# Kernel optimization log

Measured on AMD Instinct MI355X. Metric: run time of the kernel, lower is better.

Reference implementation:

```python
import jax, jax.numpy as jnp
import numpy as np

B, S, D, H = 4, 2048, 1024, 16
DH = D // H

def setup_inputs() -> dict:
    key = jax.random.key(0)
    ks = jax.random.split(key, 4)
    scale = 1.0 / np.sqrt(D)
    x = jax.random.normal(ks[0], (B, S, D), dtype=jnp.float32)
    Wq = jax.random.normal(ks[1], (D, D), dtype=jnp.float32) * scale
    Wk = jax.random.normal(ks[2], (D, D), dtype=jnp.float32) * scale
    Wv = jax.random.normal(ks[3], (D, D), dtype=jnp.float32) * scale
    bq = jnp.zeros((D,), dtype=jnp.float32)
    bk = jnp.zeros((D,), dtype=jnp.float32)
    bv = jnp.zeros((D,), dtype=jnp.float32)
    # causal mask, broadcastable to [B, H, S, S]; mask==0 positions get -inf
    mask = jnp.tril(jnp.ones((S, S), dtype=bool))[None, None, :, :]
    return {"x": x, "mask": mask, "Wq": Wq, "bq": bq, "Wk": Wk, "bk": bk, "Wv": Wv, "bv": bv}

def reference(x, mask, Wq, bq, Wk, bk, Wv, bv):
    b, s, d = x.shape
    def proj(W, bias):
        # nn.Linear: x @ W.T + b, then split heads -> [b, H, s, DH]
        y = jnp.einsum('bsd,ed->bse', x, W) + bias
        return y.reshape(b, s, H, DH).transpose(0, 2, 1, 3)
    q = proj(Wq, bq)
    k = proj(Wk, bk)
    v = proj(Wv, bv)
    scores = jnp.einsum('bhqd,bhkd->bhqk', q, k) / jnp.sqrt(jnp.float32(DH))
    scores = jnp.where(mask, scores, -jnp.inf)
    attn = jax.nn.softmax(scores, axis=-1)
    out = jnp.einsum('bhqk,bhkd->bhqd', attn, v)
    return out.transpose(0, 2, 1, 3).reshape(b, s, d)
```

## Files before the change

kernel.cpp:

```cpp
#include <hip/hip_runtime.h>
#include <hip/hip_bf16.h>
#include <stdint.h>

typedef unsigned short u16;
typedef unsigned int   u32;
typedef short bf16x8 __attribute__((ext_vector_type(8)));
typedef float f32x4  __attribute__((ext_vector_type(4)));

typedef bf16x8 __attribute__((__may_alias__)) bf16x8_a;
typedef uint4  __attribute__((__may_alias__)) uint4_a;
typedef uint2  __attribute__((__may_alias__)) uint2_a;
typedef float4 __attribute__((__may_alias__)) float4_a;

#define MFMA_BF16(a,b,c) __builtin_amdgcn_mfma_f32_16x16x32_bf16((a),(b),(c),0,0,0)
#define L2E 1.44269504088896340736f

#define SEQ 2048
#define DMODEL 1024
#define NH 16
#define DH 64

__device__ __forceinline__ u32 pack_bf2(float a, float b) {
  union { __hip_bfloat162 h; u32 u; } c;
  c.h = __float22bfloat162_rn(make_float2(a, b));
  return c.u;
}

__device__ __forceinline__ u16 f2bf(float f) {
  u32 u = __builtin_bit_cast(u32, f);
  u += 0x7FFFu + ((u >> 16) & 1u);
  return (u16)(u >> 16);
}

__device__ __forceinline__ void gl_lds16(const u16* g, u16* l) {
  __builtin_amdgcn_global_load_lds(
      (const __attribute__((address_space(1))) void*)g,
      (__attribute__((address_space(3))) void*)l, 16, 0, 0);
}

__global__ __launch_bounds__(256) void cvt_x_bf16(
    const float* __restrict__ s, u16* __restrict__ d, int n8)
{
  int i = blockIdx.x * 256 + threadIdx.x;
  const int stride = gridDim.x * 256;
  for (; i < n8; i += stride) {
    const float4_a* p = (const float4_a*)(s + (size_t)i * 8);
    float4 a = p[0], b = p[1];
    uint4 o;
    o.x = pack_bf2(a.x, a.y); o.y = pack_bf2(a.z, a.w);
    o.z = pack_bf2(b.x, b.y); o.w = pack_bf2(b.z, b.w);
    *(uint4_a*)(d + (size_t)i * 8) = o;
  }
}

__global__ __launch_bounds__(256) void cvt_w_bf16(
    const float* __restrict__ wq, const float* __restrict__ wk, const float* __restrict__ wv,
    u16* __restrict__ oq, u16* __restrict__ ok, u16* __restrict__ ov)
{
  const float* s = (blockIdx.y == 0) ? wq : (blockIdx.y == 1) ? wk : wv;
  u16*         d = (blockIdx.y == 0) ? oq : (blockIdx.y == 1) ? ok : ov;
  const int i = blockIdx.x * 256 + threadIdx.x;
  const float4_a* p = (const float4_a*)(s + (size_t)i * 8);
  float4 a = p[0], b = p[1];
  uint4 o;
  o.x = pack_bf2(a.x, a.y); o.y = pack_bf2(a.z, a.w);
  o.z = pack_bf2(b.x, b.y); o.w = pack_bf2(b.z, b.w);
  *(uint4_a*)(d + (size_t)i * 8) = o;
}

__global__ __launch_bounds__(256, 4) void qkv_gemm_bf(
    const u16* __restrict__ Xb,
    const u16* __restrict__ Wqb, const u16* __restrict__ Wkb, const u16* __restrict__ Wvb,
    const float* __restrict__ Bq, const float* __restrict__ Bk, const float* __restrict__ Bv,
    u16* __restrict__ Qo, u16* __restrict__ Ko, u16* __restrict__ Vo)
{
  __shared__ u16 As[2][128 * 32];
  __shared__ u16 Bs[2][128 * 32];

  const int tid  = threadIdx.x;
  const int lane = tid & 63;
  const int wid  = tid >> 6;
  const int l16  = lane & 15;
  const int quad = lane >> 4;
  const int wm   = (wid >> 1) * 64;
  const int wn   = (wid & 1) * 64;

  const int m0 = blockIdx.x * 128;
  const int n0 = blockIdx.y * 128;
  const int pj = blockIdx.z;

  const u16*   Wb   = (pj == 0) ? Wqb : (pj == 1) ? Wkb : Wvb;
  const float* Bias = (pj == 0) ? Bq : (pj == 1) ? Bk : Bv;
  u16*         Out  = (pj == 0) ? Qo : (pj == 1) ? Ko : Vo;
  const float scale = (pj == 0) ? 0.125f : 1.0f;

  f32x4 acc[4][4];
#pragma unroll
  for (int i = 0; i < 4; i++)
#pragma unroll
    for (int j = 0; j < 4; j++) acc[i][j] = (f32x4){0.f, 0.f, 0.f, 0.f};

  const int lr = lane >> 2;
  const int lc = (lane & 3) * 8;

  const u16* Arow = Xb + (size_t)m0 * DMODEL;
  const u16* Brow = Wb + (size_t)n0 * DMODEL;

#pragma unroll
  for (int c = 0; c < 2; c++) {
    const int band = c * 64 + wid * 16;
    gl_lds16(Arow + (size_t)(band + lr) * DMODEL + lc, &As[0][band * 32]);
    gl_lds16(Brow + (size_t)(band + lr) * DMODEL + lc, &Bs[0][band * 32]);
  }

  for (int kt = 0; kt < DMODEL; kt += 32) {
    const int cur = (kt >> 5) & 1;
    __syncthreads();

    if (kt + 32 < DMODEL) {
#pragma unroll
      for (int c = 0; c < 2; c++) {
        const int band = c * 64 + wid * 16;
        gl_lds16(Arow + (size_t)(band + lr) * DMODEL + kt + 32 + lc, &As[cur ^ 1][band * 32]);
        gl_lds16(Brow + (size_t)(band + lr) * DMODEL + kt + 32 + lc, &Bs[cur ^ 1][band * 32]);
      }
    }

    bf16x8 a[4], b[4];
#pragma unroll
    for (int mt = 0; mt < 4; mt++)
      a[mt] = *(const bf16x8_a*)&As[cur][(wm + mt * 16 + l16) * 32 + quad * 8];
#pragma unroll
    for (int nt = 0; nt < 4; nt++)
      b[nt] = *(const bf16x8_a*)&Bs[cur][(wn + nt * 16 + l16) * 32 + quad * 8];
#pragma unroll
    for (int mt = 0; mt < 4; mt++)
#pragma unroll
      for (int nt = 0; nt < 4; nt++)
        acc[mt][nt] = MFMA_BF16(a[mt], b[nt], acc[mt][nt]);
  }

  if (pj == 2) {
#pragma unroll
    for (int mt = 0; mt < 4; mt++) {
#pragma unroll
      for (int nt = 0; nt < 4; nt++) {
        const int n = n0 + wn + nt * 16 + l16;
        const float bias = Bias[n];
        const int h = n >> 6, dh = n & 63;
        const int m = m0 + wm + mt * 16 + quad * 4;
        const int bb = m >> 11, ss = m & 2047;
        uint2 pk;
        pk.x = pack_bf2(acc[mt][nt][0] + bias, acc[mt][nt][1] + bias);
        pk.y = pack_bf2(acc[mt][nt][2] + bias, acc[mt][nt][3] + bias);
        *(uint2_a*)&Out[((size_t)(bb * NH + h) * DH + dh) * SEQ + ss] = pk;
      }
    }
  } else {
#pragma unroll
    for (int mt = 0; mt < 4; mt++) {
#pragma unroll
      for (int nt = 0; nt < 4; nt++) {
        const int n = n0 + wn + nt * 16 + l16;
        const float bias = Bias[n];
        const int h = n >> 6, dh = n & 63;
#pragma unroll
        for (int r = 0; r < 4; r++) {
          const int m = m0 + wm + mt * 16 + quad * 4 + r;
          const int bb = m >> 11, ss = m & 2047;
          Out[((((size_t)bb * NH + h) * SEQ + ss) << 6) + dh] = f2bf((acc[mt][nt][r] + bias) * scale);
        }
      }
    }
  }
}

__global__ __launch_bounds__(256, 2) void qkv_gemm(
    const float* __restrict__ X,
    const float* __restrict__ Wq, const float* __restrict__ Wk, const float* __restrict__ Wv,
    const float* __restrict__ Bq, const float* __restrict__ Bk, const float* __restrict__ Bv,
    u16* __restrict__ Qo, u16* __restrict__ Ko, u16* __restrict__ Vo)
{
  __shared__ u16 As[128 * 32];
  __shared__ u16 Bs[128 * 32];

  const int tid  = threadIdx.x;
  const int lane = tid & 63;
  const int wid  = tid >> 6;
  const int l16  = lane & 15;
  const int quad = lane >> 4;
  const int wm   = (wid >> 1) * 64;
  const int wn   = (wid & 1) * 64;

  const int m0 = blockIdx.x * 128;
  const int n0 = blockIdx.y * 128;
  const int pj = blockIdx.z;

  const float* W    = (pj == 0) ? Wq : (pj == 1) ? Wk : Wv;
  const float* Bias = (pj == 0) ? Bq : (pj == 1) ? Bk : Bv;
  u16*         Out  = (pj == 0) ? Qo : (pj == 1) ? Ko : Vo;
  const float scale = (pj == 0) ? 0.125f : 1.0f;

  f32x4 acc[4][4];
#pragma unroll
  for (int i = 0; i < 4; i++)
#pragma unroll
    for (int j = 0; j < 4; j++) acc[i][j] = (f32x4){0.f, 0.f, 0.f, 0.f};

  float4 gX[4], gW[4];
#pragma unroll
  for (int i = 0; i < 4; i++) {
    const int ch = i * 256 + tid;
    const int r = ch >> 3, c = ch & 7;
    gX[i] = *(const float4_a*)(X + (size_t)(m0 + r) * DMODEL + c * 4);
    gW[i] = *(const float4_a*)(W + (size_t)(n0 + r) * DMODEL + c * 4);
  }

  for (int kt = 0; kt < DMODEL; kt += 32) {
    __syncthreads();
#pragma unroll
    for (int i = 0; i < 4; i++) {
      const int ch = i * 256 + tid;
      const int r = ch >> 3, c = ch & 7;
      uint2 xp, wp;
      xp.x = pack_bf2(gX[i].x, gX[i].y);  xp.y = pack_bf2(gX[i].z, gX[i].w);
      wp.x = pack_bf2(gW[i].x, gW[i].y);  wp.y = pack_bf2(gW[i].z, gW[i].w);
      *(uint2_a*)&As[r * 32 + c * 4] = xp;
      *(uint2_a*)&Bs[r * 32 + c * 4] = wp;
    }
    __syncthreads();

    if (kt + 32 < DMODEL) {
#pragma unroll
      for (int i = 0; i < 4; i++) {
        const int ch = i * 256 + tid;
        const int r = ch >> 3, c = ch & 7;
        gX[i] = *(const float4_a*)(X + (size_t)(m0 + r) * DMODEL + kt + 32 + c * 4);
        gW[i] = *(const float4_a*)(W + (size_t)(n0 + r) * DMODEL + kt + 32 + c * 4);
      }
    }

    bf16x8 a[4], b[4];
#pragma unroll
    for (int mt = 0; mt < 4; mt++)
      a[mt] = *(const bf16x8_a*)&As[(wm + mt * 16 + l16) * 32 + quad * 8];
#pragma unroll
    for (int nt = 0; nt < 4; nt++)
      b[nt] = *(const bf16x8_a*)&Bs[(wn + nt * 16 + l16) * 32 + quad * 8];
#pragma unroll
    for (int mt = 0; mt < 4; mt++)
#pragma unroll
      for (int nt = 0; nt < 4; nt++)
        acc[mt][nt] = MFMA_BF16(a[mt], b[nt], acc[mt][nt]);
  }

  if (pj == 2) {
#pragma unroll
    for (int mt = 0; mt < 4; mt++) {
#pragma unroll
      for (int nt = 0; nt < 4; nt++) {
        const int n = n0 + wn + nt * 16 + l16;
        const float bias = Bias[n];
        const int h = n >> 6, dh = n & 63;
        const int m = m0 + wm + mt * 16 + quad * 4;
        const int bb = m >> 11, ss = m & 2047;
        uint2 pk;
        pk.x = pack_bf2(acc[mt][nt][0] + bias, acc[mt][nt][1] + bias);
        pk.y = pack_bf2(acc[mt][nt][2] + bias, acc[mt][nt][3] + bias);
        *(uint2_a*)&Out[((size_t)(bb * NH + h) * DH + dh) * SEQ + ss] = pk;
      }
    }
  } else {
#pragma unroll
    for (int mt = 0; mt < 4; mt++) {
#pragma unroll
      for (int nt = 0; nt < 4; nt++) {
        const int n = n0 + wn + nt * 16 + l16;
        const float bias = Bias[n];
        const int h = n >> 6, dh = n & 63;
#pragma unroll
        for (int r = 0; r < 4; r++) {
          const int m = m0 + wm + mt * 16 + quad * 4 + r;
          const int bb = m >> 11, ss = m & 2047;
          Out[((((size_t)bb * NH + h) * SEQ + ss) << 6) + dh] = f2bf((acc[mt][nt][r] + bias) * scale);
        }
      }
    }
  }
}

__global__ __launch_bounds__(256, 4) void flash_attn(
    const u16* __restrict__ Q, const u16* __restrict__ K, const u16* __restrict__ VT,
    float* __restrict__ O)
{
  __shared__ u16 Ks[64 * 72];
  __shared__ u16 VTs[64 * 72];
  __shared__ u16 Ps[4 * 32 * 72];

  const int tid  = threadIdx.x;
  const int lane = tid & 63;
  const int wid  = tid >> 6;
  const int l16  = lane & 15;
  const int quad = lane >> 4;

  const int idx = blockIdx.x;
  const int qt  = 15 - (idx >> 6);
  const int bh  = idx & 63;
  const int bb = bh >> 4, hh = bh & 15;
  const int qbase = qt * 128;

  const u16* Qh = Q  + (size_t)bh * (SEQ * DH);
  const u16* Kh = K  + (size_t)bh * (SEQ * DH);
  const u16* Vh = VT + (size_t)bh * (DH * SEQ);

#pragma unroll
  for (int i = 0; i < 4; i++) {
    const int ch = i * 256 + tid;
    const int r = ch >> 3, c = ch & 7;
    *(uint4_a*)&Ps[r * 72 + c * 8] = *(const uint4_a*)(Qh + (size_t)(qbase + r) * DH + c * 8);
  }
  __syncthreads();

  u16* Pw = &Ps[wid * 32 * 72];
  bf16x8 qf[2][2];
#pragma unroll
  for (int ct = 0; ct < 2; ct++)
#pragma unroll
    for (int ks = 0; ks < 2; ks++)
      qf[ct][ks] = *(const bf16x8_a*)&Pw[(ct * 16 + l16) * 72 + ks * 32 + quad * 8];

  f32x4 o[4][2];
#pragma unroll
  for (int dt = 0; dt < 4; dt++)
#pragma unroll
    for (int ct = 0; ct < 2; ct++) o[dt][ct] = (f32x4){0.f, 0.f, 0.f, 0.f};

  float mold[2] = {-1e30f, -1e30f};
  float lsum[2] = {0.f, 0.f};

  const int jmax = 2 * qt + 1;

  uint4 gK[2], gV[2];
#pragma unroll
  for (int i = 0; i < 2; i++) {
    const int ch = i * 256 + tid;
    gK[i] = *(const uint4_a*)(Kh + (size_t)(ch >> 3) * DH + (ch & 7) * 8);
    gV[i] = *(const uint4_a*)(Vh + (size_t)(ch >> 3) * SEQ + (ch & 7) * 8);
  }

  for (int j = 0; j <= jmax; j++) {
    __syncthreads();
#pragma unroll
    for (int i = 0; i < 2; i++) {
      const int ch = i * 256 + tid;
      *(uint4_a*)&Ks[(ch >> 3) * 72 + (ch & 7) * 8]  = gK[i];
      *(uint4_a*)&VTs[(ch >> 3) * 72 + (ch & 7) * 8] = gV[i];
    }
    __syncthreads();

    if (j < jmax) {
      const int kb2 = (j + 1) * 64;
#pragma unroll
      for (int i = 0; i < 2; i++) {
        const int ch = i * 256 + tid;
        gK[i] = *(const uint4_a*)(Kh + (size_t)(kb2 + (ch >> 3)) * DH + (ch & 7) * 8);
        gV[i] = *(const uint4_a*)(Vh + (size_t)(ch >> 3) * SEQ + kb2 + (ch & 7) * 8);
      }
    }

    f32x4 s[4][2];
#pragma unroll
    for (int rt = 0; rt < 4; rt++) {
      bf16x8 ka0 = *(const bf16x8_a*)&Ks[(rt * 16 + l16) * 72 + 0 + quad * 8];
      bf16x8 ka1 = *(const bf16x8_a*)&Ks[(rt * 16 + l16) * 72 + 32 + quad * 8];
#pragma unroll
      for (int ct = 0; ct < 2; ct++) {
        f32x4 c = (f32x4){0.f, 0.f, 0.f, 0.f};
        c = MFMA_BF16(ka0, qf[ct][0], c);
        c = MFMA_BF16(ka1, qf[ct][1], c);
        s[rt][ct] = c;
      }
    }

    if (j >= (qt << 1)) {
      const int kvb = j * 64;
#pragma unroll
      for (int rt = 0; rt < 4; rt++)
#pragma unroll
        for (int ct = 0; ct < 2; ct++) {
          const int ql = qbase + wid * 32 + ct * 16 + l16;
#pragma unroll
          for (int r = 0; r < 4; r++) {
            const int kvg = kvb + rt * 16 + quad * 4 + r;
            if (kvg > ql) s[rt][ct][r] = -1e30f;
          }
        }
    }

#pragma unroll
    for (int ct = 0; ct < 2; ct++) {
      float mt = -1e30f;
#pragma unroll
      for (int rt = 0; rt < 4; rt++)
#pragma unroll
        for (int r = 0; r < 4; r++) mt = fmaxf(mt, s[rt][ct][r]);
      mt = fmaxf(mt, __shfl_xor(mt, 16));
      mt = fmaxf(mt, __shfl_xor(mt, 32));
      const float mnew = fmaxf(mold[ct], mt);
      const float a = __builtin_amdgcn_exp2f((mold[ct] - mnew) * L2E);
      float ls = 0.f;
#pragma unroll
      for (int rt = 0; rt < 4; rt++)
#pragma unroll
        for (int r = 0; r < 4; r++) {
          const float p = __builtin_amdgcn_exp2f((s[rt][ct][r] - mnew) * L2E);
          s[rt][ct][r] = p;
          ls += p;
        }
      ls += __shfl_xor(ls, 16);
      ls += __shfl_xor(ls, 32);
      lsum[ct] = lsum[ct] * a + ls;
      mold[ct] = mnew;
#pragma unroll
      for (int dt = 0; dt < 4; dt++)
#pragma unroll
        for (int r = 0; r < 4; r++) o[dt][ct][r] *= a;
    }

#pragma unroll
    for (int rt = 0; rt < 4; rt++) {
#pragma unroll
      for (int ct = 0; ct < 2; ct++) {
        uint2 pk;
        pk.x = pack_bf2(s[rt][ct][0], s[rt][ct][1]);
        pk.y = pack_bf2(s[rt][ct][2], s[rt][ct][3]);
        *(uint2_a*)&Pw[(ct * 16 + l16) * 72 + rt * 16 + quad * 4] = pk;
      }
    }
    asm volatile("s_waitcnt lgkmcnt(0)" ::: "memory");

#pragma unroll
    for (int ks2 = 0; ks2 < 2; ks2++) {
      bf16x8 vt[4], pb[2];
#pragma unroll
      for (int dt = 0; dt < 4; dt++)
        vt[dt] = *(const bf16x8_a*)&VTs[(dt * 16 + l16) * 72 + ks2 * 32 + quad * 8];
#pragma unroll
      for (int ct = 0; ct < 2; ct++)
        pb[ct] = *(const bf16x8_a*)&Pw[(ct * 16 + l16) * 72 + ks2 * 32 + quad * 8];
#pragma unroll
      for (int dt = 0; dt < 4; dt++)
#pragma unroll
        for (int ct = 0; ct < 2; ct++)
          o[dt][ct] = MFMA_BF16(vt[dt], pb[ct], o[dt][ct]);
    }
  }

#pragma unroll
  for (int ct = 0; ct < 2; ct++) {
    const float inv = 1.0f / lsum[ct];
    const int qg = qbase + wid * 32 + ct * 16 + l16;
    float* orow = O + (size_t)((size_t)bb * SEQ + qg) * DMODEL + hh * 64;
#pragma unroll
    for (int dt = 0; dt < 4; dt++) {
      float4 v4;
      v4.x = o[dt][ct][0] * inv;  v4.y = o[dt][ct][1] * inv;
      v4.z = o[dt][ct][2] * inv;  v4.w = o[dt][ct][3] * inv;
      *(float4_a*)&orow[dt * 16 + quad * 4] = v4;
    }
  }
}

__global__ void paintf(float* out, int n, float v) {
  int i = blockIdx.x * 256 + threadIdx.x;
  if (i < n) out[i] = v;
}

extern "C" void kernel_launch(void* const* d_in, const int* in_sizes, int n_in,
                              void* d_out, int out_size, void* d_ws, size_t ws_size,
                              hipStream_t stream) {
  float* out = (float*)d_out;

  const size_t elems  = (size_t)4 * SEQ * DMODEL;
  const size_t welems = (size_t)DMODEL * DMODEL;
  const size_t need_old = 3 * elems * sizeof(u16);
  const size_t need_new = (4 * elems + 3 * welems) * sizeof(u16);

  if (ws_size < need_old) {
    paintf<<<(out_size + 255) / 256, 256, 0, stream>>>(out, out_size, 3.0e38f);
    return;
  }

  const float* x  = (const float*)d_in[0];
  const float* Wq = (const float*)d_in[2];
  const float* bq = (const float*)d_in[3];
  const float* Wk = (const float*)d_in[4];
  const float* bk = (const float*)d_in[5];
  const float* Wv = (const float*)d_in[6];
  const float* bv = (const float*)d_in[7];

  u16* q = (u16*)d_ws;
  u16* k = q + elems;
  u16* v = k + elems;

  if (ws_size >= need_new) {
    u16* xb  = v + elems;
    u16* wqb = xb + elems;
    u16* wkb = wqb + welems;
    u16* wvb = wkb + welems;
    cvt_x_bf16<<<2048, 256, 0, stream>>>(x, xb, (int)(elems / 8));
    cvt_w_bf16<<<dim3(512, 3), 256, 0, stream>>>(Wq, Wk, Wv, wqb, wkb, wvb);
    qkv_gemm_bf<<<dim3(64, 8, 3), 256, 0, stream>>>(xb, wqb, wkb, wvb, bq, bk, bv, q, k, v);
  } else {
    qkv_gemm<<<dim3(64, 8, 3), 256, 0, stream>>>(x, Wq, Wk, Wv, bq, bk, bv, q, k, v);
  }

  flash_attn<<<1024, 256, 0, stream>>>(q, k, v, out);
}
```

Before: 289.1 us.

## Deepen projection GEMM prefetch, reorder attention tile schedule, add lazy softmax rescale

The projection GEMM now prefetches two K-tiles ahead, using explicit vmcnt waits and raw s_barriers in place of __syncthreads, so global-to-LDS loads overlap more compute. The flash-attention block-to-q-tile mapping is changed to interleave heavy and light causal tiles across waves, aiming for better load balance. The online softmax skips the max update and accumulator rescale unless the new row max exceeds the old one by more than a threshold, and the max and sum reductions are written as trees. Skipping the rescale lets exp values exceed 1 (bounded by e^8), which slightly risks precision. The hand-written waitcnt counts must match the number of outstanding loads exactly.

```diff
diff --git a/kernel.cpp b/kernel.cpp
--- a/kernel.cpp
+++ b/kernel.cpp
@@ -106,33 +106,49 @@
   const u16* Arow = Xb + (size_t)m0 * DMODEL;
   const u16* Brow = Wb + (size_t)n0 * DMODEL;
 
+  const int NT = DMODEL / 32;
+
 #pragma unroll
   for (int c = 0; c < 2; c++) {
     const int band = c * 64 + wid * 16;
-    gl_lds16(Arow + (size_t)(band + lr) * DMODEL + lc, &As[0][band * 32]);
-    gl_lds16(Brow + (size_t)(band + lr) * DMODEL + lc, &Bs[0][band * 32]);
-  }
-
-  for (int kt = 0; kt < DMODEL; kt += 32) {
-    const int cur = (kt >> 5) & 1;
-    __syncthreads();
-
-    if (kt + 32 < DMODEL) {
+    gl_lds16(Arow + (size_t)(band + lr) * DMODEL + 0 + lc, &As[0][band * 32]);
+    gl_lds16(Brow + (size_t)(band + lr) * DMODEL + 0 + lc, &Bs[0][band * 32]);
+  }
+#pragma unroll
+  for (int c = 0; c < 2; c++) {
+    const int band = c * 64 + wid * 16;
+    gl_lds16(Arow + (size_t)(band + lr) * DMODEL + 32 + lc, &As[1][band * 32]);
+    gl_lds16(Brow + (size_t)(band + lr) * DMODEL + 32 + lc, &Bs[1][band * 32]);
+  }
+
+  for (int t = 0; t < NT; ++t) {
+    const int cur = t & 1;
+    if (t < NT - 1) asm volatile("s_waitcnt vmcnt(4)" ::: "memory");
+    else            asm volatile("s_waitcnt vmcnt(0)" ::: "memory");
+    __builtin_amdgcn_s_barrier();
+
+    bf16x8 a[4], b[4];
+#pragma unroll
+    for (int mt = 0; mt < 4; mt++)
+      a[mt] = *(const bf16x8_a*)&As[cur][(wm + mt * 16 + l16) * 32 + quad * 8];
+#pragma unroll
+    for (int nt = 0; nt < 4; nt++)
+      b[nt] = *(const bf16x8_a*)&Bs[cur][(wn + nt * 16 + l16) * 32 + quad * 8];
+
+    asm volatile("s_waitcnt lgkmcnt(0)" ::: "memory");
+    __builtin_amdgcn_sched_barrier(0);
+    __builtin_amdgcn_s_barrier();
+
+    if (t + 2 < NT) {
+      const int kt2 = (t + 2) * 32;
 #pragma unroll
       for (int c = 0; c < 2; c++) {
         const int band = c * 64 + wid * 16;
-        gl_lds16(Arow + (size_t)(band + lr) * DMODEL + kt + 32 + lc, &As[cur ^ 1][band * 32]);
-        gl_lds16(Brow + (size_t)(band + lr) * DMODEL + kt + 32 + lc, &Bs[cur ^ 1][band * 32]);
-      }
-    }
-
-    bf16x8 a[4], b[4];
-#pragma unroll
-    for (int mt = 0; mt < 4; mt++)
-      a[mt] = *(const bf16x8_a*)&As[cur][(wm + mt * 16 + l16) * 32 + quad * 8];
-#pragma unroll
-    for (int nt = 0; nt < 4; nt++)
-      b[nt] = *(const bf16x8_a*)&Bs[cur][(wn + nt * 16 + l16) * 32 + quad * 8];
+        gl_lds16(Arow + (size_t)(band + lr) * DMODEL + kt2 + lc, &As[cur][band * 32]);
+        gl_lds16(Brow + (size_t)(band + lr) * DMODEL + kt2 + lc, &Bs[cur][band * 32]);
+      }
+    }
+
 #pragma unroll
     for (int mt = 0; mt < 4; mt++)
 #pragma unroll
@@ -304,7 +320,8 @@
   const int quad = lane >> 4;
 
   const int idx = blockIdx.x;
-  const int qt  = 15 - (idx >> 6);
+  const int y = idx >> 6, g = y >> 2, r4 = y & 3;
+  const int qt = (g & 1) ? ((g == 1 ? 0 : 4) + r4) : ((g == 0 ? 15 : 11) - r4);
   const int bh  = idx & 63;
   const int bb = bh >> 4, hh = bh & 15;
   const int qbase = qt * 128;
@@ -399,32 +416,40 @@
 
 #pragma unroll
     for (int ct = 0; ct < 2; ct++) {
-      float mt = -1e30f;
-#pragma unroll
-      for (int rt = 0; rt < 4; rt++)
-#pragma unroll
-        for (int r = 0; r < 4; r++) mt = fmaxf(mt, s[rt][ct][r]);
+      float m0_ = fmaxf(fmaxf(s[0][ct][0], s[0][ct][1]), fmaxf(s[0][ct][2], s[0][ct][3]));
+      float m1_ = fmaxf(fmaxf(s[1][ct][0], s[1][ct][1]), fmaxf(s[1][ct][2], s[1][ct][3]));
+      float m2_ = fmaxf(fmaxf(s[2][ct][0], s[2][ct][1]), fmaxf(s[2][ct][2], s[2][ct][3]));
+      float m3_ = fmaxf(fmaxf(s[3][ct][0], s[3][ct][1]), fmaxf(s[3][ct][2], s[3][ct][3]));
+      float mt = fmaxf(fmaxf(m0_, m1_), fmaxf(m2_, m3_));
       mt = fmaxf(mt, __shfl_xor(mt, 16));
       mt = fmaxf(mt, __shfl_xor(mt, 32));
-      const float mnew = fmaxf(mold[ct], mt);
-      const float a = __builtin_amdgcn_exp2f((mold[ct] - mnew) * L2E);
-      float ls = 0.f;
+
+      if (!__all(mt - mold[ct] <= 8.0f)) {
+        const float mnew = fmaxf(mold[ct], mt);
+        const float a = __builtin_amdgcn_exp2f((mold[ct] - mnew) * L2E);
+        lsum[ct] *= a;
+        mold[ct] = mnew;
+#pragma unroll
+        for (int dt = 0; dt < 4; dt++)
+#pragma unroll
+          for (int r = 0; r < 4; r++) o[dt][ct][r] *= a;
+      }
+      const float mref = mold[ct];
+
 #pragma unroll
       for (int rt = 0; rt < 4; rt++)
 #pragma unroll
-        for (int r = 0; r < 4; r++) {
-          const float p = __builtin_amdgcn_exp2f((s[rt][ct][r] - mnew) * L2E);
-          s[rt][ct][r] = p;
-          ls += p;
-        }
+        for (int r = 0; r < 4; r++)
+          s[rt][ct][r] = __builtin_amdgcn_exp2f((s[rt][ct][r] - mref) * L2E);
+
+      float t0 = (s[0][ct][0] + s[0][ct][1]) + (s[0][ct][2] + s[0][ct][3]);
+      float t1 = (s[1][ct][0] + s[1][ct][1]) + (s[1][ct][2] + s[1][ct][3]);
+      float t2 = (s[2][ct][0] + s[2][ct][1]) + (s[2][ct][2] + s[2][ct][3]);
+      float t3 = (s[3][ct][0] + s[3][ct][1]) + (s[3][ct][2] + s[3][ct][3]);
+      float ls = (t0 + t1) + (t2 + t3);
       ls += __shfl_xor(ls, 16);
       ls += __shfl_xor(ls, 32);
-      lsum[ct] = lsum[ct] * a + ls;
-      mold[ct] = mnew;
-#pragma unroll
-      for (int dt = 0; dt < 4; dt++)
-#pragma unroll
-        for (int r = 0; r < 4; r++) o[dt][ct][r] *= a;
+      lsum[ct] += ls;
     }
 
 #pragma unroll
```

Measured after the change: 287.5 us. Within noise of the previous version (-0.5%).
